# Optimization experiments

Hardware: AMD Instinct MI355X
Metric: run time of the kernel (lower is better)

Reference implementation:

```python
import jax, jax.numpy as jnp
from jax import lax
import numpy as np

B, N, C = 4, 16384, 64
M_POINT, K_SAMPLE = 1024, 32
RADIUS = 0.5
LN_EPS = 1e-5
CP = C + 3  # grouped channels with use_xyz


def _fps(xyz, m):
    """D-FPS: furthest point sampling on Euclidean coords. xyz (B,N,3) -> (B,m) int32."""
    b, n, _ = xyz.shape
    min_d = jnp.full((b, n), 1e10, xyz.dtype)
    pt0 = xyz[:, 0]  # CUDA FPS starts from index 0

    def step(carry, _):
        md, last = carry
        d = jnp.sum((xyz - last[:, None, :]) ** 2, axis=-1)  # (B,N)
        md = jnp.minimum(md, d)
        idx = jnp.argmax(md, axis=1)  # (B,)
        nxt = jnp.take_along_axis(xyz, idx[:, None, None], axis=1)[:, 0]
        return (md, nxt), idx.astype(jnp.int32)

    _, idxs = lax.scan(step, (min_d, pt0), None, length=m - 1)  # (m-1,B)
    return jnp.concatenate([jnp.zeros((1, b), jnp.int32), idxs], axis=0).T  # (B,m)


def _ball_query(xyz, new_xyz, radius, k):
    """First k neighbors (by original index) within radius; pad with first hit. -> (B,M,k)."""
    b, n, _ = xyz.shape
    d2 = jnp.sum((new_xyz[:, :, None, :] - xyz[:, None, :, :]) ** 2, -1)  # (B,M,N)
    scores = jnp.where(d2 <= radius * radius, jnp.arange(n, dtype=jnp.int32), n)
    neg_top, _ = lax.top_k(-scores, k)  # k smallest scores = first k in-radius indices
    idx = -neg_top  # (B,M,k), ascending
    idx = jnp.where(idx < n, idx, idx[..., :1])  # pad invalid slots with first hit
    return idx


def setup_inputs() -> dict:
    key = jax.random.key(0)
    ks = jax.random.split(key, 8)
    points_xyz = jax.random.uniform(ks[0], (B, N, 3)) * 2.0 - 1.0
    features = jax.random.normal(ks[1], (B, C, N))
    prompt_emb = jax.random.normal(ks[2], (1, M_POINT, 2)) * 0.02
    proj_w = jax.random.normal(ks[3], (CP, 2)) * 0.5
    proj_b = jnp.zeros((CP,))
    ln_g = jnp.ones((CP,))
    ln_b = jnp.zeros((CP,))
    pw_w = jax.random.normal(ks[4], (M_POINT, CP)) * 0.05
    pw_b = jnp.zeros((M_POINT,))
    w0 = jax.random.normal(ks[5], (128, CP)) / np.sqrt(CP)
    b0 = jnp.zeros((128,))
    w1 = jax.random.normal(ks[6], (256, 128)) / np.sqrt(128.0)
    b1 = jnp.zeros((256,))
    return dict(points_xyz=points_xyz, features=features, prompt_emb=prompt_emb,
                proj_w=proj_w, proj_b=proj_b, ln_g=ln_g, ln_b=ln_b,
                pw_w=pw_w, pw_b=pw_b, w0=w0, b0=b0, w1=w1, b1=b1)


def reference(points_xyz, features, prompt_emb, proj_w, proj_b, ln_g, ln_b,
              pw_w, pw_b, w0, b0, w1, b1):
    # sample centers (D-FPS)
    indices = _fps(points_xyz, M_POINT)                                   # (B,M)
    new_xyz = jnp.take_along_axis(points_xyz, indices[:, :, None], axis=1)  # (B,M,3)
    # ball-query grouping + gather
    idx = _ball_query(points_xyz, new_xyz, RADIUS, K_SAMPLE)              # (B,M,K)
    gx = jax.vmap(lambda p, i: p[i])(points_xyz, idx)                     # (B,M,K,3)
    gx = gx - new_xyz[:, :, None, :]                                      # relative xyz
    gf = jax.vmap(lambda f, i: f[:, i])(features, idx)                    # (B,C,M,K)
    g = jnp.concatenate([jnp.transpose(gx, (0, 3, 1, 2)), gf], axis=1)    # (B,C+3,M,K)
    # incorporate_prompt
    emb = g.mean(axis=(-2, -1))                                           # (B,C+3)
    pw = jax.nn.softmax(emb @ pw_w.T + pw_b, axis=1)                      # (B,M)
    pe = prompt_emb @ proj_w.T + proj_b                                   # (1,M,C+3)
    mu = pe.mean(-1, keepdims=True)
    var = ((pe - mu) ** 2).mean(-1, keepdims=True)
    pe = (pe - mu) * lax.rsqrt(var + LN_EPS) * ln_g + ln_b
    pe = jax.nn.gelu(pe, approximate=False)                               # (1,M,C+3)
    g = g + pe[0].T[None, :, :, None] * pw[:, None, :, None]              # (B,C+3,M,K)
    # shared MLP (1x1 conv) + ReLU
    h = jax.nn.relu(jnp.einsum('oc,bcmk->bomk', w0, g) + b0[:, None, None])
    h = jax.nn.relu(jnp.einsum('oc,bcmk->bomk', w1, h) + b1[:, None, None])
    # max pool over neighbors K
    pooled = h.max(axis=-1)                                               # (B,256,M)
    return new_xyz, pooled, indices
```

## Files before the change

### kernel.cpp

```cpp
#include <hip/hip_runtime.h>
#include <hip/hip_bf16.h>

#define NB   4
#define NPTS 16384
#define NC   64
#define NM   1024
#define NK   32
#define NCP  67
#define RAD2 0.25f

#define OFF_W0T     0u
#define OFF_W1T     8576u
#define OFF_NEWXYZ  41344u
#define OFF_IDXBALL 53632u
#define OFF_CNT     184704u
#define OFF_EMB     250240u
#define OFF_PW      250624u
#define OFF_PE      254720u

#define OUT_NEWXYZ 0u
#define OUT_POOLED 12288u
#define OUT_IDX    1060864u

__global__ __launch_bounds__(256) void k_prepw(const float* __restrict__ w0,
                                               const float* __restrict__ w1,
                                               float* __restrict__ w0t,
                                               float* __restrict__ w1t) {
  int t = blockIdx.x * 256 + threadIdx.x;
  if (t < 128 * NCP) { int o = t / NCP, c = t % NCP; w0t[c * 128 + o] = w0[t]; }
  if (t < 256 * 128) { int o2 = t / 128, o = t % 128; w1t[o * 256 + o2] = w1[t]; }
}

__global__ __launch_bounds__(512, 1) void k_fps(const float* __restrict__ xyz,
                                                float* __restrict__ newxyz,
                                                float* __restrict__ out) {
  const int b = blockIdx.x;
  const int t = threadIdx.x;
  const float* xb = xyz + (size_t)b * NPTS * 3;
  __shared__ float2 sxy[NPTS];
  __shared__ unsigned long long c_key[2][8];
  __shared__ float c_z[2][8];
  float px[32], py[32], pz[32], md[32];
#pragma unroll
  for (int i = 0; i < 32; ++i) {
    int p = t + 512 * i;
    px[i] = xb[p * 3 + 0];
    py[i] = xb[p * 3 + 1];
    pz[i] = xb[p * 3 + 2];
    sxy[p] = make_float2(px[i], py[i]);
    md[i] = 1e10f;
  }
  float lx = xb[0], ly = xb[1], lz = xb[2];
  if (t == 0) {
    newxyz[(size_t)b * NM * 3 + 0] = lx;
    newxyz[(size_t)b * NM * 3 + 1] = ly;
    newxyz[(size_t)b * NM * 3 + 2] = lz;
    out[OUT_NEWXYZ + (size_t)b * NM * 3 + 0] = lx;
    out[OUT_NEWXYZ + (size_t)b * NM * 3 + 1] = ly;
    out[OUT_NEWXYZ + (size_t)b * NM * 3 + 2] = lz;
    out[OUT_IDX + b * NM] = 0.0f;
  }
  __syncthreads();
  const int wid = t >> 6;
  for (int s = 1; s < NM; ++s) {
    float best = -1.0f;
    int   bidx = 0;
    float bz   = 0.0f;
#pragma unroll
    for (int i = 0; i < 32; ++i) {
      float dx = __fsub_rn(px[i], lx);
      float dy = __fsub_rn(py[i], ly);
      float dz = __fsub_rn(pz[i], lz);
      float d2 = __fadd_rn(__fadd_rn(__fmul_rn(dx, dx), __fmul_rn(dy, dy)),
                           __fmul_rn(dz, dz));
      float m0 = fminf(md[i], d2);
      md[i] = m0;
      bool gt = m0 > best;
      best = gt ? m0 : best;
      bidx = gt ? (t + 512 * i) : bidx;
      bz   = gt ? pz[i] : bz;
    }
    unsigned long long key =
        ((unsigned long long)__float_as_uint(best) << 32) |
        (unsigned long long)(unsigned)(16383 - bidx);
    unsigned long long kr = key;
#pragma unroll
    for (int off = 1; off < 64; off <<= 1) {
      unsigned long long ok = __shfl_xor(kr, off);
      kr = ok > kr ? ok : kr;
    }
    const int pp = s & 1;
    if ((t & 63) == 0) c_key[pp][wid] = kr;
    if (key == kr) c_z[pp][wid] = bz;
    __syncthreads();
    unsigned long long k = c_key[pp][t & 7];
#pragma unroll
    for (int off = 1; off < 8; off <<= 1) {
      unsigned long long ok = __shfl_xor(k, off);
      k = ok > k ? ok : k;
    }
    const int bi = 16383 - (int)(unsigned)(k & 0xffffffffull);
    float2 cxy = sxy[bi];
    lx = cxy.x;
    ly = cxy.y;
    lz = c_z[pp][(bi >> 6) & 7];
    if (t == 0) {
      newxyz[((size_t)b * NM + s) * 3 + 0] = lx;
      newxyz[((size_t)b * NM + s) * 3 + 1] = ly;
      newxyz[((size_t)b * NM + s) * 3 + 2] = lz;
      out[OUT_NEWXYZ + ((size_t)b * NM + s) * 3 + 0] = lx;
      out[OUT_NEWXYZ + ((size_t)b * NM + s) * 3 + 1] = ly;
      out[OUT_NEWXYZ + ((size_t)b * NM + s) * 3 + 2] = lz;
      out[OUT_IDX + b * NM + s] = (float)bi;
    }
  }
}

__global__ __launch_bounds__(256) void k_ball(const float* __restrict__ xyz,
                                              const float* __restrict__ newxyz,
                                              int* __restrict__ idxball,
                                              int* __restrict__ cnt,
                                              float* __restrict__ emb) {
  __shared__ int s_idx[4][NK];
  const int lane = threadIdx.x & 63, wid = threadIdx.x >> 6;
  const int gid = blockIdx.x * 4 + wid;
  const int b = gid >> 10;
  const float* xb = xyz + (size_t)b * NPTS * 3;
  const float cx = newxyz[gid * 3 + 0];
  const float cy = newxyz[gid * 3 + 1];
  const float cz = newxyz[gid * 3 + 2];
  int total = 0;
  for (int base = 0; base < NPTS && total < NK; base += 64) {
    int n = base + lane;
    float dx = __fsub_rn(xb[n * 3 + 0], cx);
    float dy = __fsub_rn(xb[n * 3 + 1], cy);
    float dz = __fsub_rn(xb[n * 3 + 2], cz);
    float d2 = __fadd_rn(__fadd_rn(__fmul_rn(dx, dx), __fmul_rn(dy, dy)),
                         __fmul_rn(dz, dz));
    bool hit = d2 <= RAD2;
    unsigned long long mask = __ballot(hit);
    int pos = total + (int)__popcll(mask & ((1ull << lane) - 1ull));
    if (hit && pos < NK) s_idx[wid][pos] = n;
    total += (int)__popcll(mask);
  }
  int tt = total < NK ? total : NK;
  if (lane >= tt && lane < NK) s_idx[wid][lane] = s_idx[wid][0];
  int v = 0;
  if (lane < NK) {
    v = s_idx[wid][lane];
    idxball[(size_t)gid * NK + lane] = v;
    atomicAdd(&cnt[b * NPTS + v], 1);
  }
  float sx = 0.f, sy = 0.f, sz = 0.f;
  if (lane < NK) { sx = xb[v * 3 + 0]; sy = xb[v * 3 + 1]; sz = xb[v * 3 + 2]; }
#pragma unroll
  for (int off = 1; off < 64; off <<= 1) {
    sx += __shfl_xor(sx, off);
    sy += __shfl_xor(sy, off);
    sz += __shfl_xor(sz, off);
  }
  if (lane == 0) {
    atomicAdd(&emb[b * 96 + 0], sx - 32.0f * cx);
    atomicAdd(&emb[b * 96 + 1], sy - 32.0f * cy);
    atomicAdd(&emb[b * 96 + 2], sz - 32.0f * cz);
  }
}

__global__ __launch_bounds__(256) void k_embfeat(const float* __restrict__ feat,
                                                 const int* __restrict__ cnt,
                                                 float* __restrict__ emb) {
  const int c = blockIdx.x, b = blockIdx.y;
  const float* f = feat + ((size_t)b * NC + c) * NPTS;
  const int* ct = cnt + b * NPTS;
  float acc = 0.f;
  for (int n = threadIdx.x; n < NPTS; n += 256)
    acc = fmaf((float)ct[n], f[n], acc);
  __shared__ float red[4];
#pragma unroll
  for (int off = 1; off < 64; off <<= 1) acc += __shfl_xor(acc, off);
  if ((threadIdx.x & 63) == 0) red[threadIdx.x >> 6] = acc;
  __syncthreads();
  if (threadIdx.x == 0)
    emb[b * 96 + 3 + c] = red[0] + red[1] + red[2] + red[3];
}

__global__ __launch_bounds__(64) void k_pe(const float* __restrict__ prompt,
                                           const float* __restrict__ projw,
                                           const float* __restrict__ projb,
                                           const float* __restrict__ lng,
                                           const float* __restrict__ lnb,
                                           float* __restrict__ pe) {
  const int m = blockIdx.x, lane = threadIdx.x;
  const float p0 = prompt[m * 2 + 0], p1 = prompt[m * 2 + 1];
  const int c1 = lane, c2 = lane + 64;
  float v1 = p0 * projw[c1 * 2 + 0] + p1 * projw[c1 * 2 + 1] + projb[c1];
  float v2 = 0.f;
  if (c2 < NCP) v2 = p0 * projw[c2 * 2 + 0] + p1 * projw[c2 * 2 + 1] + projb[c2];
  float s = v1 + ((c2 < NCP) ? v2 : 0.f);
#pragma unroll
  for (int off = 1; off < 64; off <<= 1) s += __shfl_xor(s, off);
  float mu = s * (1.0f / 67.0f);
  float d1 = v1 - mu;
  float d2v = (c2 < NCP) ? (v2 - mu) : 0.f;
  float q = d1 * d1 + d2v * d2v;
#pragma unroll
  for (int off = 1; off < 64; off <<= 1) q += __shfl_xor(q, off);
  float inv = 1.0f / sqrtf(q * (1.0f / 67.0f) + 1e-5f);
  {
    float y = d1 * inv * lng[c1] + lnb[c1];
    pe[m * NCP + c1] = 0.5f * y * (1.0f + erff(y * 0.70710678118654752f));
  }
  if (c2 < NCP) {
    float y = (v2 - mu) * inv * lng[c2] + lnb[c2];
    pe[m * NCP + c2] = 0.5f * y * (1.0f + erff(y * 0.70710678118654752f));
  }
}

__global__ __launch_bounds__(1024) void k_pw(const float* __restrict__ emb,
                                             const float* __restrict__ pww,
                                             const float* __restrict__ pwb,
                                             float* __restrict__ pw) {
  const int b = blockIdx.x, m = threadIdx.x;
  __shared__ float se[NCP];
  __shared__ float red[16];
  __shared__ float bcast;
  if (m < NCP) se[m] = emb[b * 96 + m] * (1.0f / 32768.0f);
  __syncthreads();
  float acc = pwb[m];
  for (int c = 0; c < NCP; ++c) acc = fmaf(se[c], pww[m * NCP + c], acc);
  float mx = acc;
#pragma unroll
  for (int off = 1; off < 64; off <<= 1) mx = fmaxf(mx, __shfl_xor(mx, off));
  if ((m & 63) == 0) red[m >> 6] = mx;
  __syncthreads();
  if (m == 0) {
    float v = red[0];
    for (int w = 1; w < 16; ++w) v = fmaxf(v, red[w]);
    bcast = v;
  }
  __syncthreads();
  float e = expf(acc - bcast);
  float ssum = e;
#pragma unroll
  for (int off = 1; off < 64; off <<= 1) ssum += __shfl_xor(ssum, off);
  if ((m & 63) == 0) red[m >> 6] = ssum;
  __syncthreads();
  if (m == 0) {
    float v = 0.f;
    for (int w = 0; w < 16; ++w) v += red[w];
    bcast = v;
  }
  __syncthreads();
  pw[b * NM + m] = e / bcast;
}

__global__ __launch_bounds__(256) void k_main(const float* __restrict__ feat,
                                              const float* __restrict__ xyz,
                                              const float* __restrict__ newxyz,
                                              const int* __restrict__ idxball,
                                              const float* __restrict__ pe,
                                              const float* __restrict__ pwbuf,
                                              const float* __restrict__ w0t,
                                              const float* __restrict__ b0,
                                              const float* __restrict__ w1t,
                                              const float* __restrict__ b1,
                                              float* __restrict__ out) {
  __shared__ __align__(16) float g[NCP * 36];
  __shared__ __align__(16) float h0[128 * 36];
  __shared__ int s_idx[NK];
  __shared__ float spe[NCP];
  const int bid = blockIdx.x;
  const int b = bid >> 10, m = bid & 1023;
  const int t = threadIdx.x;
  const float pwv = pwbuf[bid];
  if (t < NK) {
    int n = idxball[(size_t)bid * NK + t];
    n = n < 0 ? 0 : (n > NPTS - 1 ? NPTS - 1 : n);
    s_idx[t] = n;
  }
  if (t < NCP) spe[t] = pe[m * NCP + t] * pwv;
  __syncthreads();
  for (int e = t; e < NK * NC; e += 256) {
    int k = e >> 6, c = e & 63;
    int n = s_idx[k];
    g[(3 + c) * 36 + k] = feat[((size_t)b * NC + c) * NPTS + n] + spe[3 + c];
  }
  if (t < 96) {
    int k = t & 31, d = t >> 5;
    int n = s_idx[k];
    float cv = newxyz[bid * 3 + d];
    g[d * 36 + k] = (xyz[((size_t)b * NPTS + n) * 3 + d] - cv) + spe[d];
  }
  __syncthreads();
  {
    const int o = t & 127, kb = (t >> 7) * 16;
    float acc[16];
    float bb = b0[o];
#pragma unroll
    for (int j = 0; j < 16; ++j) acc[j] = bb;
    for (int c = 0; c < NCP; ++c) {
      float w = w0t[c * 128 + o];
      const float4* gp = reinterpret_cast<const float4*>(&g[c * 36 + kb]);
#pragma unroll
      for (int qq = 0; qq < 4; ++qq) {
        float4 gv = gp[qq];
        acc[qq * 4 + 0] = fmaf(w, gv.x, acc[qq * 4 + 0]);
        acc[qq * 4 + 1] = fmaf(w, gv.y, acc[qq * 4 + 1]);
        acc[qq * 4 + 2] = fmaf(w, gv.z, acc[qq * 4 + 2]);
        acc[qq * 4 + 3] = fmaf(w, gv.w, acc[qq * 4 + 3]);
      }
    }
    float4* hp = reinterpret_cast<float4*>(&h0[o * 36 + kb]);
#pragma unroll
    for (int qq = 0; qq < 4; ++qq) {
      float4 hv;
      hv.x = fmaxf(acc[qq * 4 + 0], 0.f);
      hv.y = fmaxf(acc[qq * 4 + 1], 0.f);
      hv.z = fmaxf(acc[qq * 4 + 2], 0.f);
      hv.w = fmaxf(acc[qq * 4 + 3], 0.f);
      hp[qq] = hv;
    }
  }
  __syncthreads();
  {
    const int o2 = t;
    float acc[32];
    float bb = b1[o2];
#pragma unroll
    for (int j = 0; j < 32; ++j) acc[j] = bb;
    for (int o = 0; o < 128; ++o) {
      float w = w1t[o * 256 + o2];
      const float4* hp = reinterpret_cast<const float4*>(&h0[o * 36]);
#pragma unroll
      for (int qq = 0; qq < 8; ++qq) {
        float4 hv = hp[qq];
        acc[qq * 4 + 0] = fmaf(w, hv.x, acc[qq * 4 + 0]);
        acc[qq * 4 + 1] = fmaf(w, hv.y, acc[qq * 4 + 1]);
        acc[qq * 4 + 2] = fmaf(w, hv.z, acc[qq * 4 + 2]);
        acc[qq * 4 + 3] = fmaf(w, hv.w, acc[qq * 4 + 3]);
      }
    }
    float mx = 0.f;
#pragma unroll
    for (int k = 0; k < 32; ++k) mx = fmaxf(mx, acc[k]);
    out[OUT_POOLED + ((size_t)(b * 256 + o2)) * NM + m] = mx;
  }
}

extern "C" void kernel_launch(void* const* d_in, const int* in_sizes, int n_in,
                              void* d_out, int out_size, void* d_ws, size_t ws_size,
                              hipStream_t stream) {
  const float* xyz    = (const float*)d_in[0];
  const float* feat   = (const float*)d_in[1];
  const float* prompt = (const float*)d_in[2];
  const float* projw  = (const float*)d_in[3];
  const float* projb  = (const float*)d_in[4];
  const float* lng    = (const float*)d_in[5];
  const float* lnb    = (const float*)d_in[6];
  const float* pww    = (const float*)d_in[7];
  const float* pwb    = (const float*)d_in[8];
  const float* w0     = (const float*)d_in[9];
  const float* b0     = (const float*)d_in[10];
  const float* w1     = (const float*)d_in[11];
  const float* b1     = (const float*)d_in[12];
  float* ws = (float*)d_ws;
  float* out = (float*)d_out;

  float* w0t     = ws + OFF_W0T;
  float* w1t     = ws + OFF_W1T;
  float* nxyz    = ws + OFF_NEWXYZ;
  int*   idxball = (int*)(ws + OFF_IDXBALL);
  int*   cnt     = (int*)(ws + OFF_CNT);
  float* emb     = ws + OFF_EMB;
  float* pwv     = ws + OFF_PW;
  float* pev     = ws + OFF_PE;

  hipMemsetAsync(cnt, 0, NB * NPTS * sizeof(int), stream);
  hipMemsetAsync(emb, 0, NB * 96 * sizeof(float), stream);

  k_prepw<<<128, 256, 0, stream>>>(w0, w1, w0t, w1t);
  k_fps<<<NB, 512, 0, stream>>>(xyz, nxyz, out);
  k_ball<<<NB * NM / 4, 256, 0, stream>>>(xyz, nxyz, idxball, cnt, emb);
  k_embfeat<<<dim3(NC, NB), 256, 0, stream>>>(feat, cnt, emb);
  k_pe<<<NM, 64, 0, stream>>>(prompt, projw, projb, lng, lnb, pev);
  k_pw<<<NB, 1024, 0, stream>>>(emb, pww, pwb, pwv);
  k_main<<<NB * NM, 256, 0, stream>>>(feat, xyz, nxyz, idxball, pev, pwv,
                                      w0t, b0, w1t, b1, out);
}
```

Measured before the change: 2.163 ms.

## Streamline FPS step: scalar registers, direct wave-key reduction, global coord fetch

Rewrites the FPS per-point state as 32 explicitly named scalar registers via macros and folds the index into a precomputed key offset, removing the per-step bidx/bz tracking. The cross-wave reduction now reads all eight wave keys as vector loads and takes a scalar max tree instead of a second shuffle reduction. The 128KB shared-memory xy cache and the per-wave z staging are dropped, and the selected point's coordinates are reloaded from global memory (L1/L2 cached) each step. The global reload puts a dependent memory latency on the serial 1023-step critical path in exchange for cheaper ALU and reduction work.

New measurement: 1.992 ms, median of 2. -7.9%, faster.

```diff
diff --git a/kernel.cpp b/kernel.cpp
--- a/kernel.cpp
+++ b/kernel.cpp
@@ -31,25 +31,40 @@
   if (t < 256 * 128) { int o2 = t / 128, o = t % 128; w1t[o * 256 + o2] = w1[t]; }
 }
 
+__device__ __forceinline__ unsigned long long umax64(unsigned long long a,
+                                                     unsigned long long b) {
+  return a > b ? a : b;
+}
+
+#define FPS_DECL(i) float px##i, py##i, pz##i, md##i;
+#define FPS_INIT(i) { int p = t + 512 * (i); \
+  px##i = xb[p * 3 + 0]; py##i = xb[p * 3 + 1]; pz##i = xb[p * 3 + 2]; \
+  md##i = 1e10f; }
+#define FPS_UPD(i) { \
+  float dx = __fsub_rn(px##i, lx); \
+  float dy = __fsub_rn(py##i, ly); \
+  float dz = __fsub_rn(pz##i, lz); \
+  float d2 = __fadd_rn(__fadd_rn(__fmul_rn(dx, dx), __fmul_rn(dy, dy)), \
+                       __fmul_rn(dz, dz)); \
+  float m0 = fminf(md##i, d2); \
+  md##i = m0; \
+  bool gt = m0 > best; \
+  best = gt ? m0 : best; \
+  klo  = gt ? (kbase - 512u * (i)) : klo; }
+#define FPS_REP32(M) M(0) M(1) M(2) M(3) M(4) M(5) M(6) M(7) \
+  M(8) M(9) M(10) M(11) M(12) M(13) M(14) M(15) \
+  M(16) M(17) M(18) M(19) M(20) M(21) M(22) M(23) \
+  M(24) M(25) M(26) M(27) M(28) M(29) M(30) M(31)
+
 __global__ __launch_bounds__(512, 1) void k_fps(const float* __restrict__ xyz,
                                                 float* __restrict__ newxyz,
                                                 float* __restrict__ out) {
   const int b = blockIdx.x;
   const int t = threadIdx.x;
   const float* xb = xyz + (size_t)b * NPTS * 3;
-  __shared__ float2 sxy[NPTS];
-  __shared__ unsigned long long c_key[2][8];
-  __shared__ float c_z[2][8];
-  float px[32], py[32], pz[32], md[32];
-#pragma unroll
-  for (int i = 0; i < 32; ++i) {
-    int p = t + 512 * i;
-    px[i] = xb[p * 3 + 0];
-    py[i] = xb[p * 3 + 1];
-    pz[i] = xb[p * 3 + 2];
-    sxy[p] = make_float2(px[i], py[i]);
-    md[i] = 1e10f;
-  }
+  __shared__ __align__(16) unsigned long long c_key[2][8];
+  FPS_REP32(FPS_DECL)
+  FPS_REP32(FPS_INIT)
   float lx = xb[0], ly = xb[1], lz = xb[2];
   if (t == 0) {
     newxyz[(size_t)b * NM * 3 + 0] = lx;
@@ -62,28 +77,14 @@
   }
   __syncthreads();
   const int wid = t >> 6;
+  const unsigned kbase = 16383u - (unsigned)t;
   for (int s = 1; s < NM; ++s) {
     float best = -1.0f;
-    int   bidx = 0;
-    float bz   = 0.0f;
-#pragma unroll
-    for (int i = 0; i < 32; ++i) {
-      float dx = __fsub_rn(px[i], lx);
-      float dy = __fsub_rn(py[i], ly);
-      float dz = __fsub_rn(pz[i], lz);
-      float d2 = __fadd_rn(__fadd_rn(__fmul_rn(dx, dx), __fmul_rn(dy, dy)),
-                           __fmul_rn(dz, dz));
-      float m0 = fminf(md[i], d2);
-      md[i] = m0;
-      bool gt = m0 > best;
-      best = gt ? m0 : best;
-      bidx = gt ? (t + 512 * i) : bidx;
-      bz   = gt ? pz[i] : bz;
-    }
-    unsigned long long key =
+    unsigned klo = 0u;
+    FPS_REP32(FPS_UPD)
+    unsigned long long kr =
         ((unsigned long long)__float_as_uint(best) << 32) |
-        (unsigned long long)(unsigned)(16383 - bidx);
-    unsigned long long kr = key;
+        (unsigned long long)klo;
 #pragma unroll
     for (int off = 1; off < 64; off <<= 1) {
       unsigned long long ok = __shfl_xor(kr, off);
@@ -91,19 +92,16 @@
     }
     const int pp = s & 1;
     if ((t & 63) == 0) c_key[pp][wid] = kr;
-    if (key == kr) c_z[pp][wid] = bz;
     __syncthreads();
-    unsigned long long k = c_key[pp][t & 7];
-#pragma unroll
-    for (int off = 1; off < 8; off <<= 1) {
-      unsigned long long ok = __shfl_xor(k, off);
-      k = ok > k ? ok : k;
-    }
+    const ulonglong2* ck = reinterpret_cast<const ulonglong2*>(&c_key[pp][0]);
+    ulonglong2 k01 = ck[0], k23 = ck[1], k45 = ck[2], k67 = ck[3];
+    unsigned long long k =
+        umax64(umax64(umax64(k01.x, k01.y), umax64(k23.x, k23.y)),
+               umax64(umax64(k45.x, k45.y), umax64(k67.x, k67.y)));
     const int bi = 16383 - (int)(unsigned)(k & 0xffffffffull);
-    float2 cxy = sxy[bi];
-    lx = cxy.x;
-    ly = cxy.y;
-    lz = c_z[pp][(bi >> 6) & 7];
+    lx = xb[bi * 3 + 0];
+    ly = xb[bi * 3 + 1];
+    lz = xb[bi * 3 + 2];
     if (t == 0) {
       newxyz[((size_t)b * NM + s) * 3 + 0] = lx;
       newxyz[((size_t)b * NM + s) * 3 + 1] = ly;
```
